# Performance work log

Hardware: AMD Instinct MI355X
Metric: run time of the kernel (lower is better)

The kernel has to match this reference:

```python
import jax, jax.numpy as jnp
import numpy as np

B, S, H, E = 4, 4096, 4096, 64
EPS = 1e-6


def setup_inputs() -> dict:
    key = jax.random.key(0)
    k1, k2 = jax.random.split(key)
    hidden_states = jax.random.normal(k1, (B, S, H), dtype=jnp.float32)
    gate_w = jax.random.normal(k2, (E, H), dtype=jnp.float32) * 0.02
    return {"hidden_states": hidden_states, "gate_w": gate_w, "C": 512}


def reference(hidden_states, gate_w, C):
    b, s, h = hidden_states.shape
    e = gate_w.shape[0]
    flat = hidden_states.reshape(-1, h)                    # [BS, H]
    logits = jnp.einsum('th,eh->te', flat, gate_w)          # [BS, E]
    # deterministic=True -> no noise added
    probs = jax.nn.softmax(logits, axis=-1)                 # [BS, E]
    # expert-choice: each expert picks top-C tokens
    _, topC_idx = jax.lax.top_k(logits.T, C)                # [E, C] token indices
    routing_map = jnp.zeros_like(logits).at[
        topC_idx, jnp.arange(e)[:, None]].set(1.0)          # [BS, E]
    # normalize_weights=True
    probs = probs * routing_map
    probs = probs / (probs.sum(axis=-1, keepdims=True) + EPS)
    # aux losses (torch .std() is unbiased -> ddof=1)
    importance = probs.sum(axis=0)                          # [E]
    imp_loss = (jnp.std(importance, ddof=1) / (importance.mean() + EPS)) ** 2
    load = routing_map.sum(axis=0)                          # [E]
    load_loss = (jnp.std(load, ddof=1) / (load.mean() + EPS)) ** 2
    aux_loss = imp_loss + load_loss
    return (probs.reshape(b, s, e), routing_map.reshape(b, s, e), aux_loss)
```

## Files before the change

### kernel.cpp

```cpp
#include <hip/hip_runtime.h>
#include <hip/hip_bf16.h>

#define BS 16384
#define HDIM 4096
#define NE 64
#define KC 64
#define TILE_T 64
#define CAP 512
#define DELTA 2e-3f

__device__ inline unsigned f2key(float f) {
    unsigned u = __float_as_uint(f);
    return (u & 0x80000000u) ? ~u : (u | 0x80000000u);
}
__device__ inline float key2f(unsigned k) {
    unsigned u = (k & 0x80000000u) ? (k ^ 0x80000000u) : ~k;
    return __uint_as_float(u);
}

__global__ __launch_bounds__(1024, 4) void k1_gemm(const float* __restrict__ A,
                                                   const float* __restrict__ W,
                                                   float* __restrict__ Lg,
                                                   unsigned* __restrict__ KeyT) {
    __shared__ __align__(16) float smem[2 * KC * 68];
    float (*As)[68] = (float(*)[68])smem;
    float (*Ws)[68] = (float(*)[68])(smem + KC * 68);

    const int tid = threadIdx.x;
    const int T0  = blockIdx.x * TILE_T;

    const int kq  = tid & 15;
    const int row = tid >> 4;

    const int qt   = tid >> 8;
    const int htid = tid & 255;
    const int tx   = htid & 15;
    const int ty   = htid >> 4;

    float  cacc[4][4];
    double acc[4][4];
#pragma unroll
    for (int i = 0; i < 4; ++i)
#pragma unroll
        for (int j = 0; j < 4; ++j) { cacc[i][j] = 0.f; acc[i][j] = 0.0; }

    float4 ra = *(const float4*)&A[(size_t)(T0 + row) * HDIM + 4 * kq];
    float4 rw = *(const float4*)&W[(size_t)row * HDIM + 4 * kq];

    const int NCHUNK = HDIM / KC;
    for (int c = 0; c < NCHUNK; ++c) {
        __syncthreads();
        *(float4*)&As[row][4 * kq] = ra;
        Ws[4 * kq + 0][row] = rw.x;
        Ws[4 * kq + 1][row] = rw.y;
        Ws[4 * kq + 2][row] = rw.z;
        Ws[4 * kq + 3][row] = rw.w;
        __syncthreads();
        if (c + 1 < NCHUNK) {
            const int c0 = (c + 1) * KC;
            ra = *(const float4*)&A[(size_t)(T0 + row) * HDIM + c0 + 4 * kq];
            rw = *(const float4*)&W[(size_t)row * HDIM + c0 + 4 * kq];
        }
        const int kb = qt * 16;
#pragma unroll
        for (int k4 = 0; k4 < 4; ++k4) {
            const int k0 = kb + 4 * k4;
            float4 a0 = *(const float4*)&As[4 * ty + 0][k0];
            float4 a1 = *(const float4*)&As[4 * ty + 1][k0];
            float4 a2 = *(const float4*)&As[4 * ty + 2][k0];
            float4 a3 = *(const float4*)&As[4 * ty + 3][k0];
            float4 w0 = *(const float4*)&Ws[k0 + 0][4 * tx];
            float4 w1 = *(const float4*)&Ws[k0 + 1][4 * tx];
            float4 w2 = *(const float4*)&Ws[k0 + 2][4 * tx];
            float4 w3 = *(const float4*)&Ws[k0 + 3][4 * tx];
            const float* ap[4] = {(const float*)&a0, (const float*)&a1,
                                  (const float*)&a2, (const float*)&a3};
            const float* wp[4] = {(const float*)&w0, (const float*)&w1,
                                  (const float*)&w2, (const float*)&w3};
#pragma unroll
            for (int s = 0; s < 4; ++s)
#pragma unroll
                for (int i = 0; i < 4; ++i)
#pragma unroll
                    for (int j = 0; j < 4; ++j)
                        cacc[i][j] = fmaf(ap[i][s], wp[s][j], cacc[i][j]);
        }
        if ((c & 3) == 3) {
#pragma unroll
            for (int i = 0; i < 4; ++i)
#pragma unroll
                for (int j = 0; j < 4; ++j) { acc[i][j] += (double)cacc[i][j]; cacc[i][j] = 0.f; }
        }
    }

    double* dbuf = (double*)smem;
    __syncthreads();
    if (qt == 3) {
#pragma unroll
        for (int i = 0; i < 4; ++i)
#pragma unroll
            for (int j = 0; j < 4; ++j) dbuf[htid * 16 + i * 4 + j] = acc[i][j];
    }
    __syncthreads();
    if (qt == 2) {
#pragma unroll
        for (int i = 0; i < 4; ++i)
#pragma unroll
            for (int j = 0; j < 4; ++j) dbuf[htid * 16 + i * 4 + j] += acc[i][j];
    }
    __syncthreads();
    if (qt == 1) {
#pragma unroll
        for (int i = 0; i < 4; ++i)
#pragma unroll
            for (int j = 0; j < 4; ++j) dbuf[htid * 16 + i * 4 + j] += acc[i][j];
    }
    __syncthreads();
    if (qt == 0) {
        float f[4][4];
#pragma unroll
        for (int i = 0; i < 4; ++i)
#pragma unroll
            for (int j = 0; j < 4; ++j)
                f[i][j] = (float)(acc[i][j] + dbuf[htid * 16 + i * 4 + j]);
#pragma unroll
        for (int i = 0; i < 4; ++i) {
            const int t = T0 + 4 * ty + i;
            float4 o = {f[i][0], f[i][1], f[i][2], f[i][3]};
            *(float4*)&Lg[(size_t)t * NE + 4 * tx] = o;
        }
#pragma unroll
        for (int j = 0; j < 4; ++j) {
            const int e = 4 * tx + j;
            uint4 kv = {f2key(f[0][j]), f2key(f[1][j]), f2key(f[2][j]), f2key(f[3][j])};
            *(uint4*)&KeyT[(size_t)e * BS + T0 + 4 * ty] = kv;
        }
    }
}

__global__ __launch_bounds__(1024) void k2_select(const unsigned* __restrict__ KeyT,
                                                  const int* __restrict__ Cptr,
                                                  unsigned* __restrict__ khi_g,
                                                  int* __restrict__ needed_g,
                                                  int* __restrict__ ncand_g,
                                                  int* __restrict__ cand_g,
                                                  unsigned* __restrict__ win_g) {
    const int e = blockIdx.x;
    const int tid = threadIdx.x;
    const unsigned* col = KeyT + (size_t)e * BS;
    const int C = *Cptr;

    __shared__ int hist[256];
    __shared__ int sfx[256];
    __shared__ unsigned s_pref;
    __shared__ int s_rem, s_nc, s_nd;

    if (tid == 0) { s_pref = 0u; s_rem = C; s_nc = 0; s_nd = 0; }
    for (int i = tid; i < CAP; i += 1024) win_g[(size_t)e * CAP + i] = 0u;
    __syncthreads();

    for (int p = 3; p >= 0; --p) {
        if (tid < 256) hist[tid] = 0;
        __syncthreads();
        const int shift = 8 * p;
        const unsigned maskhi = (p == 3) ? 0u : (0xFFFFFFFFu << (shift + 8));
        const unsigned pref = s_pref;
        const int rem = s_rem;
        for (int i = 0; i < BS / 1024; ++i) {
            const unsigned k = col[i * 1024 + tid];
            if ((k & maskhi) == pref) atomicAdd(&hist[(k >> shift) & 255u], 1);
        }
        __syncthreads();
        if (tid < 256) sfx[tid] = hist[tid];
        __syncthreads();
        for (int off = 1; off < 256; off <<= 1) {
            int v = 0;
            if (tid < 256 && tid + off < 256) v = sfx[tid + off];
            __syncthreads();
            if (tid < 256) sfx[tid] += v;
            __syncthreads();
        }
        if (tid < 256) {
            const int Sd = sfx[tid];
            const int Sd1 = (tid == 255) ? 0 : sfx[tid + 1];
            if (Sd >= rem && Sd1 < rem) {
                s_pref = pref | ((unsigned)tid << shift);
                s_rem = rem - Sd1;
            }
        }
        __syncthreads();
    }

    const float vT = key2f(s_pref);
    const unsigned khi = f2key(vT + DELTA);
    const unsigned klo = f2key(vT - DELTA);

    for (int i = 0; i < BS / 1024; ++i) {
        const int t = i * 1024 + tid;
        const unsigned k = col[t];
        if (k > khi) atomicAdd(&s_nd, 1);
        else if (k >= klo) {
            const int pos = atomicAdd(&s_nc, 1);
            if (pos < CAP) cand_g[(size_t)e * CAP + pos] = t;
        }
    }
    __syncthreads();
    if (tid == 0) {
        khi_g[e] = khi;
        needed_g[e] = C - s_nd;
        ncand_g[e] = (s_nc < CAP) ? s_nc : CAP;
    }
}

__global__ __launch_bounds__(256) void k2b_resolve(const float* __restrict__ A,
                                                   const float* __restrict__ W,
                                                   const int* __restrict__ needed_g,
                                                   const int* __restrict__ ncand_g,
                                                   const int* __restrict__ cand_g,
                                                   unsigned* __restrict__ win_g) {
    const int e = blockIdx.x;
    const int tid = threadIdx.x;
    int n = ncand_g[e]; if (n > CAP) n = CAP;
    int need = needed_g[e];
    if (need > n) need = n;
    if (need < 0) need = 0;

    __shared__ double sval[CAP];
    __shared__ int sidx[CAP];
    __shared__ unsigned char chosen[CAP];
    __shared__ double wred[4];

    for (int i = tid; i < CAP; i += 256) {
        sidx[i] = (i < n) ? cand_g[(size_t)e * CAP + i] : 0;
        chosen[i] = 0;
    }
    __syncthreads();

    const float* Wr = W + (size_t)e * HDIM;
    for (int c = 0; c < n; ++c) {
        const int t = sidx[c];
        const float* Ar = A + (size_t)t * HDIM;
        double ps = 0.0;
#pragma unroll
        for (int j = 0; j < HDIM / 256; ++j)
            ps += (double)Ar[j * 256 + tid] * (double)Wr[j * 256 + tid];
#pragma unroll
        for (int off = 32; off; off >>= 1) ps += __shfl_xor(ps, off);
        if ((tid & 63) == 0) wred[tid >> 6] = ps;
        __syncthreads();
        if (tid == 0) sval[c] = wred[0] + wred[1] + wred[2] + wred[3];
        __syncthreads();
    }

    if (tid == 0) {
        for (int s = 0; s < need; ++s) {
            int best = -1;
            for (int c = 0; c < n; ++c) {
                if (chosen[c]) continue;
                if (best < 0 || sval[c] > sval[best] ||
                    (sval[c] == sval[best] && sidx[c] < sidx[best]))
                    best = c;
            }
            chosen[best] = 1;
            const int t = sidx[best];
            win_g[(size_t)e * CAP + (t >> 5)] |= (1u << (t & 31));
        }
    }
}

__global__ __launch_bounds__(256) void k3_softmax(const float* __restrict__ Lg,
                                                  const unsigned* __restrict__ khi_g,
                                                  const unsigned* __restrict__ win_g,
                                                  float* __restrict__ probs,
                                                  float* __restrict__ out_map,
                                                  double* __restrict__ imp_partial) {
    const int tid = threadIdx.x;
    const int w = tid >> 6;
    const int e = tid & 63;
    const int b = blockIdx.x;

    __shared__ unsigned skhi[64];
    __shared__ double buf[4][64];
    if (tid < 64) skhi[tid] = khi_g[tid];
    __syncthreads();

    double accim = 0.0;
    for (int it = 0; it < 16; ++it) {
        const int t = b * 64 + it * 4 + w;
        const float x = Lg[(size_t)t * NE + e];
        const unsigned key = f2key(x);
        float m;
        if (key > skhi[e]) m = 1.f;
        else m = ((win_g[(size_t)e * CAP + (t >> 5)] >> (t & 31)) & 1u) ? 1.f : 0.f;

        float mx = x;
#pragma unroll
        for (int off = 32; off; off >>= 1) mx = fmaxf(mx, __shfl_xor(mx, off));
        const float ev = expf(x - mx);
        float s = ev;
#pragma unroll
        for (int off = 32; off; off >>= 1) s += __shfl_xor(s, off);
        const float p = ev / s;
        const float pm = p * m;
        float s2 = pm;
#pragma unroll
        for (int off = 32; off; off >>= 1) s2 += __shfl_xor(s2, off);
        const float o = pm / (s2 + 1e-6f);
        probs[(size_t)t * NE + e] = o;
        out_map[(size_t)t * NE + e] = m;
        accim += (double)o;
    }
    buf[w][e] = accim;
    __syncthreads();
    if (w == 0)
        imp_partial[(size_t)b * NE + e] = buf[0][e] + buf[1][e] + buf[2][e] + buf[3][e];
}

__global__ __launch_bounds__(64) void k4_aux(const double* __restrict__ imp_partial,
                                             float* __restrict__ out_aux) {
    const int e = threadIdx.x;
    double s = 0.0;
    for (int b = 0; b < 256; ++b) s += imp_partial[(size_t)b * NE + e];
    __shared__ double imp[64];
    imp[e] = s;
    __syncthreads();
    if (e == 0) {
        double mean = 0.0;
        for (int i = 0; i < 64; ++i) mean += imp[i];
        mean /= 64.0;
        double var = 0.0;
        for (int i = 0; i < 64; ++i) { const double d = imp[i] - mean; var += d * d; }
        var /= 63.0;
        const double denom = mean + 1e-6;
        out_aux[0] = (float)(var / (denom * denom));
    }
}

extern "C" void kernel_launch(void* const* d_in, const int* in_sizes, int n_in,
                              void* d_out, int out_size, void* d_ws, size_t ws_size,
                              hipStream_t stream) {
    const float* A = (const float*)d_in[0];
    const float* W = (const float*)d_in[1];
    const int* Cptr = (const int*)d_in[2];

    float* out_probs = (float*)d_out;
    float* out_map   = out_probs + (size_t)BS * NE;
    float* out_aux   = out_map + (size_t)BS * NE;

    char* wsb = (char*)d_ws;
    float*    Lg      = (float*)wsb;
    unsigned* KeyT    = (unsigned*)(wsb + (4u << 20));
    unsigned* khi_g   = (unsigned*)(wsb + (8u << 20));
    int*      needed  = (int*)(wsb + (8u << 20) + 1024);
    int*      ncand   = (int*)(wsb + (8u << 20) + 2048);
    int*      cand    = (int*)(wsb + (8u << 20) + 4096);
    unsigned* winners = (unsigned*)(wsb + (8u << 20) + (256u << 10));
    double*   imp     = (double*)(wsb + (8u << 20) + (512u << 10));

    k1_gemm<<<BS / TILE_T, 1024, 0, stream>>>(A, W, Lg, KeyT);
    k2_select<<<NE, 1024, 0, stream>>>(KeyT, Cptr, khi_g, needed, ncand, cand, winners);
    k2b_resolve<<<NE, 256, 0, stream>>>(A, W, needed, ncand, cand, winners);
    k3_softmax<<<256, 256, 0, stream>>>(Lg, khi_g, winners, out_probs, out_map, imp);
    k4_aux<<<1, 64, 0, stream>>>(imp, out_aux);
}
```

Measured before the change: 486.0 us.

## Use split-bf16 MFMA gating GEMM with fused key histogram selection

Replaces the fp32/fp64 FMA gating GEMM with bf16 MFMA instructions, splitting A and W into high and low bf16 parts (three products) to keep near-fp32 accuracy. A new init kernel pre-splits W and zeroes a 16-bit-prefix histogram. The GEMM fills that histogram atomically so selection needs a single prefix-scan pass instead of four radix passes over the keys. The resolve, softmax and aux kernels are also restructured: warp-parallel candidates, no max subtraction in softmax, and atomic importance accumulation. The risks are lower logit precision near the top-C threshold, where the fp64 resolve path has to cover the ties, possible overflow of expf without the max shift, and contention on the global histogram atomics.

```diff
diff --git a/kernel.cpp b/kernel.cpp
--- a/kernel.cpp
+++ b/kernel.cpp
@@ -5,9 +5,14 @@
 #define HDIM 4096
 #define NE 64
 #define KC 64
-#define TILE_T 64
+#define TT 32
 #define CAP 512
 #define DELTA 2e-3f
+#define NBIN 65536
+
+typedef __bf16 bf16x8 __attribute__((ext_vector_type(8)));
+typedef float f32x4 __attribute__((ext_vector_type(4)));
+union Frag { uint4 q; bf16x8 v; };
 
 __device__ inline unsigned f2key(float f) {
     unsigned u = __float_as_uint(f);
@@ -17,193 +22,205 @@
     unsigned u = (k & 0x80000000u) ? (k ^ 0x80000000u) : ~k;
     return __uint_as_float(u);
 }
-
-__global__ __launch_bounds__(1024, 4) void k1_gemm(const float* __restrict__ A,
-                                                   const float* __restrict__ W,
-                                                   float* __restrict__ Lg,
-                                                   unsigned* __restrict__ KeyT) {
-    __shared__ __align__(16) float smem[2 * KC * 68];
-    float (*As)[68] = (float(*)[68])smem;
-    float (*Ws)[68] = (float(*)[68])(smem + KC * 68);
+__device__ inline unsigned pack_hi(float a, float b) {
+    return (__float_as_uint(a) >> 16) | (__float_as_uint(b) & 0xFFFF0000u);
+}
+__device__ inline float bf16_resid(float a) {
+    return a - __uint_as_float(__float_as_uint(a) & 0xFFFF0000u);
+}
+
+__global__ __launch_bounds__(256) void k0_init(const float* __restrict__ W,
+                                               unsigned short* __restrict__ Wh,
+                                               unsigned short* __restrict__ Wl,
+                                               unsigned* __restrict__ hist,
+                                               double* __restrict__ imp_g) {
+    const int b = blockIdx.x, t = threadIdx.x;
+    const size_t base = ((size_t)b * 256 + t) * 8;
+    uint4 z = {0, 0, 0, 0};
+    *(uint4*)(hist + base) = z;
+    *(uint4*)(hist + base + 4) = z;
+    if (b == 0 && t < 64) imp_g[t] = 0.0;
+    if (b < 256) {
+        const size_t f = ((size_t)b * 256 + t) * 4;
+        float4 w = *(const float4*)(W + f);
+        uint2 hh, ll;
+        hh.x = pack_hi(w.x, w.y); hh.y = pack_hi(w.z, w.w);
+        ll.x = pack_hi(bf16_resid(w.x), bf16_resid(w.y));
+        ll.y = pack_hi(bf16_resid(w.z), bf16_resid(w.w));
+        *(uint2*)(Wh + f) = hh;
+        *(uint2*)(Wl + f) = ll;
+    }
+}
+
+__global__ __launch_bounds__(256, 2) void k1_gemm(const float* __restrict__ A,
+                                                  const unsigned short* __restrict__ Wh,
+                                                  const unsigned short* __restrict__ Wl,
+                                                  float* __restrict__ Lg,
+                                                  unsigned* __restrict__ KeyT,
+                                                  unsigned* __restrict__ hist) {
+    __shared__ __align__(16) unsigned short As_h[TT][72], As_l[TT][72];
+    __shared__ __align__(16) unsigned short Ws_h[64][72], Ws_l[64][72];
 
     const int tid = threadIdx.x;
-    const int T0  = blockIdx.x * TILE_T;
-
-    const int kq  = tid & 15;
-    const int row = tid >> 4;
-
-    const int qt   = tid >> 8;
-    const int htid = tid & 255;
-    const int tx   = htid & 15;
-    const int ty   = htid >> 4;
-
-    float  cacc[4][4];
-    double acc[4][4];
-#pragma unroll
-    for (int i = 0; i < 4; ++i)
-#pragma unroll
-        for (int j = 0; j < 4; ++j) { cacc[i][j] = 0.f; acc[i][j] = 0.0; }
-
-    float4 ra = *(const float4*)&A[(size_t)(T0 + row) * HDIM + 4 * kq];
-    float4 rw = *(const float4*)&W[(size_t)row * HDIM + 4 * kq];
-
-    const int NCHUNK = HDIM / KC;
-    for (int c = 0; c < NCHUNK; ++c) {
-        __syncthreads();
-        *(float4*)&As[row][4 * kq] = ra;
-        Ws[4 * kq + 0][row] = rw.x;
-        Ws[4 * kq + 1][row] = rw.y;
-        Ws[4 * kq + 2][row] = rw.z;
-        Ws[4 * kq + 3][row] = rw.w;
-        __syncthreads();
-        if (c + 1 < NCHUNK) {
+    const int T0 = blockIdx.x * TT;
+    const int arow = tid >> 3, aseg = tid & 7;
+    const float* Ap = A + (size_t)(T0 + arow) * HDIM + aseg * 8;
+
+    const int lane = tid & 63, w = tid >> 6;
+    const int m = lane & 15, q = lane >> 4;
+    const int en = w * 16;
+
+    f32x4 acc0 = {0.f, 0.f, 0.f, 0.f}, acc1 = {0.f, 0.f, 0.f, 0.f};
+
+    float4 pa0, pa1;
+    uint4 pw[4];
+    pa0 = *(const float4*)(Ap);
+    pa1 = *(const float4*)(Ap + 4);
+#pragma unroll
+    for (int i = 0; i < 4; ++i) {
+        const int u = i * 256 + tid;
+        const unsigned short* Wm = (u >= 512) ? Wl : Wh;
+        const int r = (u >> 3) & 63, blk = u & 7;
+        pw[i] = *(const uint4*)(Wm + (size_t)r * HDIM + blk * 8);
+    }
+
+    for (int c = 0; c < HDIM / KC; ++c) {
+        __syncthreads();
+        {
+            uint4 H, L;
+            H.x = pack_hi(pa0.x, pa0.y); H.y = pack_hi(pa0.z, pa0.w);
+            H.z = pack_hi(pa1.x, pa1.y); H.w = pack_hi(pa1.z, pa1.w);
+            L.x = pack_hi(bf16_resid(pa0.x), bf16_resid(pa0.y));
+            L.y = pack_hi(bf16_resid(pa0.z), bf16_resid(pa0.w));
+            L.z = pack_hi(bf16_resid(pa1.x), bf16_resid(pa1.y));
+            L.w = pack_hi(bf16_resid(pa1.z), bf16_resid(pa1.w));
+            *(uint4*)(&As_h[arow][aseg * 8]) = H;
+            *(uint4*)(&As_l[arow][aseg * 8]) = L;
+#pragma unroll
+            for (int i = 0; i < 4; ++i) {
+                const int u = i * 256 + tid;
+                unsigned short* dst = (u >= 512) ? &Ws_l[0][0] : &Ws_h[0][0];
+                const int r = (u >> 3) & 63, blk = u & 7;
+                *(uint4*)(dst + r * 72 + blk * 8) = pw[i];
+            }
+        }
+        __syncthreads();
+        if (c + 1 < HDIM / KC) {
             const int c0 = (c + 1) * KC;
-            ra = *(const float4*)&A[(size_t)(T0 + row) * HDIM + c0 + 4 * kq];
-            rw = *(const float4*)&W[(size_t)row * HDIM + c0 + 4 * kq];
-        }
-        const int kb = qt * 16;
-#pragma unroll
-        for (int k4 = 0; k4 < 4; ++k4) {
-            const int k0 = kb + 4 * k4;
-            float4 a0 = *(const float4*)&As[4 * ty + 0][k0];
-            float4 a1 = *(const float4*)&As[4 * ty + 1][k0];
-            float4 a2 = *(const float4*)&As[4 * ty + 2][k0];
-            float4 a3 = *(const float4*)&As[4 * ty + 3][k0];
-            float4 w0 = *(const float4*)&Ws[k0 + 0][4 * tx];
-            float4 w1 = *(const float4*)&Ws[k0 + 1][4 * tx];
-            float4 w2 = *(const float4*)&Ws[k0 + 2][4 * tx];
-            float4 w3 = *(const float4*)&Ws[k0 + 3][4 * tx];
-            const float* ap[4] = {(const float*)&a0, (const float*)&a1,
-                                  (const float*)&a2, (const float*)&a3};
-            const float* wp[4] = {(const float*)&w0, (const float*)&w1,
-                                  (const float*)&w2, (const float*)&w3};
-#pragma unroll
-            for (int s = 0; s < 4; ++s)
-#pragma unroll
-                for (int i = 0; i < 4; ++i)
-#pragma unroll
-                    for (int j = 0; j < 4; ++j)
-                        cacc[i][j] = fmaf(ap[i][s], wp[s][j], cacc[i][j]);
-        }
-        if ((c & 3) == 3) {
-#pragma unroll
-            for (int i = 0; i < 4; ++i)
-#pragma unroll
-                for (int j = 0; j < 4; ++j) { acc[i][j] += (double)cacc[i][j]; cacc[i][j] = 0.f; }
-        }
-    }
-
-    double* dbuf = (double*)smem;
-    __syncthreads();
-    if (qt == 3) {
-#pragma unroll
-        for (int i = 0; i < 4; ++i)
-#pragma unroll
-            for (int j = 0; j < 4; ++j) dbuf[htid * 16 + i * 4 + j] = acc[i][j];
-    }
-    __syncthreads();
-    if (qt == 2) {
-#pragma unroll
-        for (int i = 0; i < 4; ++i)
-#pragma unroll
-            for (int j = 0; j < 4; ++j) dbuf[htid * 16 + i * 4 + j] += acc[i][j];
-    }
-    __syncthreads();
-    if (qt == 1) {
-#pragma unroll
-        for (int i = 0; i < 4; ++i)
-#pragma unroll
-            for (int j = 0; j < 4; ++j) dbuf[htid * 16 + i * 4 + j] += acc[i][j];
-    }
-    __syncthreads();
-    if (qt == 0) {
-        float f[4][4];
-#pragma unroll
-        for (int i = 0; i < 4; ++i)
-#pragma unroll
-            for (int j = 0; j < 4; ++j)
-                f[i][j] = (float)(acc[i][j] + dbuf[htid * 16 + i * 4 + j]);
-#pragma unroll
-        for (int i = 0; i < 4; ++i) {
-            const int t = T0 + 4 * ty + i;
-            float4 o = {f[i][0], f[i][1], f[i][2], f[i][3]};
-            *(float4*)&Lg[(size_t)t * NE + 4 * tx] = o;
-        }
-#pragma unroll
-        for (int j = 0; j < 4; ++j) {
-            const int e = 4 * tx + j;
-            uint4 kv = {f2key(f[0][j]), f2key(f[1][j]), f2key(f[2][j]), f2key(f[3][j])};
-            *(uint4*)&KeyT[(size_t)e * BS + T0 + 4 * ty] = kv;
+            pa0 = *(const float4*)(Ap + c0);
+            pa1 = *(const float4*)(Ap + c0 + 4);
+#pragma unroll
+            for (int i = 0; i < 4; ++i) {
+                const int u = i * 256 + tid;
+                const unsigned short* Wm = (u >= 512) ? Wl : Wh;
+                const int r = (u >> 3) & 63, blk = u & 7;
+                pw[i] = *(const uint4*)(Wm + (size_t)r * HDIM + c0 + blk * 8);
+            }
+        }
+#pragma unroll
+        for (int k2 = 0; k2 < 2; ++k2) {
+            const int ko = k2 * 32 + q * 8;
+            Frag ah0, ah1, al0, al1, bh, bl;
+            ah0.q = *(const uint4*)(&As_h[m][ko]);
+            ah1.q = *(const uint4*)(&As_h[m + 16][ko]);
+            al0.q = *(const uint4*)(&As_l[m][ko]);
+            al1.q = *(const uint4*)(&As_l[m + 16][ko]);
+            bh.q  = *(const uint4*)(&Ws_h[en + m][ko]);
+            bl.q  = *(const uint4*)(&Ws_l[en + m][ko]);
+            acc0 = __builtin_amdgcn_mfma_f32_16x16x32_bf16(ah0.v, bh.v, acc0, 0, 0, 0);
+            acc1 = __builtin_amdgcn_mfma_f32_16x16x32_bf16(ah1.v, bh.v, acc1, 0, 0, 0);
+            acc0 = __builtin_amdgcn_mfma_f32_16x16x32_bf16(al0.v, bh.v, acc0, 0, 0, 0);
+            acc1 = __builtin_amdgcn_mfma_f32_16x16x32_bf16(al1.v, bh.v, acc1, 0, 0, 0);
+            acc0 = __builtin_amdgcn_mfma_f32_16x16x32_bf16(ah0.v, bl.v, acc0, 0, 0, 0);
+            acc1 = __builtin_amdgcn_mfma_f32_16x16x32_bf16(ah1.v, bl.v, acc1, 0, 0, 0);
+        }
+    }
+
+#pragma unroll
+    for (int mt = 0; mt < 2; ++mt) {
+        f32x4 acc = mt ? acc1 : acc0;
+        const int e = en + m;
+#pragma unroll
+        for (int r = 0; r < 4; ++r) {
+            const int t = T0 + mt * 16 + q * 4 + r;
+            const float val = acc[r];
+            Lg[(size_t)t * NE + e] = val;
+            const unsigned key = f2key(val);
+            KeyT[(size_t)e * BS + t] = key;
+            atomicAdd(&hist[(size_t)e * NBIN + (key >> 16)], 1u);
         }
     }
 }
 
 __global__ __launch_bounds__(1024) void k2_select(const unsigned* __restrict__ KeyT,
+                                                  const unsigned* __restrict__ hist,
                                                   const int* __restrict__ Cptr,
                                                   unsigned* __restrict__ khi_g,
                                                   int* __restrict__ needed_g,
                                                   int* __restrict__ ncand_g,
                                                   int* __restrict__ cand_g,
                                                   unsigned* __restrict__ win_g) {
-    const int e = blockIdx.x;
-    const int tid = threadIdx.x;
+    const int e = blockIdx.x, tid = threadIdx.x;
+    const int C = *Cptr;
+    const unsigned* he = hist + (size_t)e * NBIN;
+    __shared__ int ls[1024];
+    __shared__ int s_tstar, s_after, s_B, s_nd, s_nc;
+
+    if (tid < 512) win_g[(size_t)e * 512 + tid] = 0u;
+    if (tid == 0) { s_nd = 0; s_nc = 0; s_tstar = 0; s_after = 0; s_B = 0; }
+
+    int s = 0;
+#pragma unroll
+    for (int i = 0; i < 16; ++i) {
+        uint4 v = *(const uint4*)(he + tid * 64 + i * 4);
+        s += (int)(v.x + v.y + v.z + v.w);
+    }
+    ls[tid] = s;
+    __syncthreads();
+    for (int off = 1; off < 1024; off <<= 1) {
+        int v = (tid + off < 1024) ? ls[tid + off] : 0;
+        __syncthreads();
+        ls[tid] += v;
+        __syncthreads();
+    }
+    if (ls[tid] >= C && (tid == 1023 || ls[tid + 1] < C)) {
+        s_tstar = tid;
+        s_after = (tid == 1023) ? 0 : ls[tid + 1];
+    }
+    __syncthreads();
+    const int tstar = s_tstar, after = s_after;
+    if (tid < 64) ls[tid] = (int)he[tstar * 64 + tid];
+    __syncthreads();
+    for (int off = 1; off < 64; off <<= 1) {
+        int v = 0;
+        if (tid < 64 && tid + off < 64) v = ls[tid + off];
+        __syncthreads();
+        if (tid < 64) ls[tid] += v;
+        __syncthreads();
+    }
+    if (tid < 64) {
+        const int sfx = ls[tid] + after;
+        const int nxt = ((tid == 63) ? 0 : ls[tid + 1]) + after;
+        if (sfx >= C && nxt < C) s_B = tstar * 64 + tid;
+    }
+    __syncthreads();
+    const int B = s_B;
+    const unsigned khi = (B >= 65535) ? 0xFFFFFFFFu
+                                      : f2key(key2f((unsigned)(B + 1) << 16) + DELTA);
+    const unsigned klo = f2key(key2f((unsigned)B << 16) - DELTA);
+
     const unsigned* col = KeyT + (size_t)e * BS;
-    const int C = *Cptr;
-
-    __shared__ int hist[256];
-    __shared__ int sfx[256];
-    __shared__ unsigned s_pref;
-    __shared__ int s_rem, s_nc, s_nd;
-
-    if (tid == 0) { s_pref = 0u; s_rem = C; s_nc = 0; s_nd = 0; }
-    for (int i = tid; i < CAP; i += 1024) win_g[(size_t)e * CAP + i] = 0u;
-    __syncthreads();
-
-    for (int p = 3; p >= 0; --p) {
-        if (tid < 256) hist[tid] = 0;
-        __syncthreads();
-        const int shift = 8 * p;
-        const unsigned maskhi = (p == 3) ? 0u : (0xFFFFFFFFu << (shift + 8));
-        const unsigned pref = s_pref;
-        const int rem = s_rem;
-        for (int i = 0; i < BS / 1024; ++i) {
-            const unsigned k = col[i * 1024 + tid];
-            if ((k & maskhi) == pref) atomicAdd(&hist[(k >> shift) & 255u], 1);
-        }
-        __syncthreads();
-        if (tid < 256) sfx[tid] = hist[tid];
-        __syncthreads();
-        for (int off = 1; off < 256; off <<= 1) {
-            int v = 0;
-            if (tid < 256 && tid + off < 256) v = sfx[tid + off];
-            __syncthreads();
-            if (tid < 256) sfx[tid] += v;
-            __syncthreads();
-        }
-        if (tid < 256) {
-            const int Sd = sfx[tid];
-            const int Sd1 = (tid == 255) ? 0 : sfx[tid + 1];
-            if (Sd >= rem && Sd1 < rem) {
-                s_pref = pref | ((unsigned)tid << shift);
-                s_rem = rem - Sd1;
-            }
-        }
-        __syncthreads();
-    }
-
-    const float vT = key2f(s_pref);
-    const unsigned khi = f2key(vT + DELTA);
-    const unsigned klo = f2key(vT - DELTA);
-
+    int nd_loc = 0;
     for (int i = 0; i < BS / 1024; ++i) {
         const int t = i * 1024 + tid;
         const unsigned k = col[t];
-        if (k > khi) atomicAdd(&s_nd, 1);
-        else if (k >= klo) {
-            const int pos = atomicAdd(&s_nc, 1);
-            if (pos < CAP) cand_g[(size_t)e * CAP + pos] = t;
-        }
-    }
+        nd_loc += (k > khi);
+        if (k >= klo && k <= khi) {
+            const int p = atomicAdd(&s_nc, 1);
+            if (p < CAP) cand_g[(size_t)e * CAP + p] = t;
+        }
+    }
+    atomicAdd(&s_nd, nd_loc);
     __syncthreads();
     if (tid == 0) {
         khi_g[e] = khi;
@@ -218,52 +235,36 @@
                                                    const int* __restrict__ ncand_g,
                                                    const int* __restrict__ cand_g,
                                                    unsigned* __restrict__ win_g) {
-    const int e = blockIdx.x;
-    const int tid = threadIdx.x;
+    const int e = blockIdx.x, tid = threadIdx.x, w = tid >> 6, lane = tid & 63;
     int n = ncand_g[e]; if (n > CAP) n = CAP;
-    int need = needed_g[e];
-    if (need > n) need = n;
-    if (need < 0) need = 0;
-
+    int need = needed_g[e]; if (need > n) need = n; if (need < 0) need = 0;
     __shared__ double sval[CAP];
     __shared__ int sidx[CAP];
-    __shared__ unsigned char chosen[CAP];
-    __shared__ double wred[4];
-
-    for (int i = tid; i < CAP; i += 256) {
-        sidx[i] = (i < n) ? cand_g[(size_t)e * CAP + i] : 0;
-        chosen[i] = 0;
-    }
-    __syncthreads();
-
     const float* Wr = W + (size_t)e * HDIM;
-    for (int c = 0; c < n; ++c) {
-        const int t = sidx[c];
+    for (int c = w; c < n; c += 4) {
+        const int t = cand_g[(size_t)e * CAP + c];
         const float* Ar = A + (size_t)t * HDIM;
         double ps = 0.0;
-#pragma unroll
-        for (int j = 0; j < HDIM / 256; ++j)
-            ps += (double)Ar[j * 256 + tid] * (double)Wr[j * 256 + tid];
+#pragma unroll 8
+        for (int j = 0; j < HDIM / 64; ++j)
+            ps += (double)Ar[j * 64 + lane] * (double)Wr[j * 64 + lane];
 #pragma unroll
         for (int off = 32; off; off >>= 1) ps += __shfl_xor(ps, off);
-        if ((tid & 63) == 0) wred[tid >> 6] = ps;
-        __syncthreads();
-        if (tid == 0) sval[c] = wred[0] + wred[1] + wred[2] + wred[3];
-        __syncthreads();
-    }
-
+        if (lane == 0) { sval[c] = ps; sidx[c] = t; }
+    }
+    __syncthreads();
     if (tid == 0) {
         for (int s = 0; s < need; ++s) {
             int best = -1;
             for (int c = 0; c < n; ++c) {
-                if (chosen[c]) continue;
+                if (sidx[c] < 0) continue;
                 if (best < 0 || sval[c] > sval[best] ||
                     (sval[c] == sval[best] && sidx[c] < sidx[best]))
                     best = c;
             }
-            chosen[best] = 1;
             const int t = sidx[best];
-            win_g[(size_t)e * CAP + (t >> 5)] |= (1u << (t & 31));
+            win_g[(size_t)e * 512 + (t >> 5)] |= (1u << (t & 31));
+            sidx[best] = -1;
         }
     }
 }
@@ -273,66 +274,56 @@
                                                   const unsigned* __restrict__ win_g,
                                                   float* __restrict__ probs,
                                                   float* __restrict__ out_map,
-                                                  double* __restrict__ imp_partial) {
-    const int tid = threadIdx.x;
-    const int w = tid >> 6;
-    const int e = tid & 63;
-    const int b = blockIdx.x;
-
+                                                  double* __restrict__ imp_g) {
+    const int tid = threadIdx.x, w = tid >> 6, e = tid & 63, b = blockIdx.x;
     __shared__ unsigned skhi[64];
-    __shared__ double buf[4][64];
+    __shared__ double sim[4][64];
     if (tid < 64) skhi[tid] = khi_g[tid];
     __syncthreads();
-
+    const unsigned kh = skhi[e];
     double accim = 0.0;
-    for (int it = 0; it < 16; ++it) {
-        const int t = b * 64 + it * 4 + w;
+#pragma unroll
+    for (int it = 0; it < 4; ++it) {
+        const int t = b * 16 + w * 4 + it;
         const float x = Lg[(size_t)t * NE + e];
         const unsigned key = f2key(x);
-        float m;
-        if (key > skhi[e]) m = 1.f;
-        else m = ((win_g[(size_t)e * CAP + (t >> 5)] >> (t & 31)) & 1u) ? 1.f : 0.f;
-
-        float mx = x;
-#pragma unroll
-        for (int off = 32; off; off >>= 1) mx = fmaxf(mx, __shfl_xor(mx, off));
-        const float ev = expf(x - mx);
-        float s = ev;
-#pragma unroll
-        for (int off = 32; off; off >>= 1) s += __shfl_xor(s, off);
-        const float p = ev / s;
-        const float pm = p * m;
-        float s2 = pm;
-#pragma unroll
-        for (int off = 32; off; off >>= 1) s2 += __shfl_xor(s2, off);
-        const float o = pm / (s2 + 1e-6f);
+        float mfl;
+        if (key > kh) mfl = 1.f;
+        else mfl = (float)((win_g[(size_t)e * 512 + (t >> 5)] >> (t & 31)) & 1u);
+        const float ev = expf(x);
+        const float evm = ev * mfl;
+        float s1 = ev, s2 = evm;
+#pragma unroll
+        for (int off = 32; off; off >>= 1) {
+            s1 += __shfl_xor(s1, off);
+            s2 += __shfl_xor(s2, off);
+        }
+        const float o = evm / (s2 + 1e-6f * s1);
         probs[(size_t)t * NE + e] = o;
-        out_map[(size_t)t * NE + e] = m;
+        out_map[(size_t)t * NE + e] = mfl;
         accim += (double)o;
     }
-    buf[w][e] = accim;
-    __syncthreads();
-    if (w == 0)
-        imp_partial[(size_t)b * NE + e] = buf[0][e] + buf[1][e] + buf[2][e] + buf[3][e];
-}
-
-__global__ __launch_bounds__(64) void k4_aux(const double* __restrict__ imp_partial,
+    sim[w][e] = accim;
+    __syncthreads();
+    if (w == 0) atomicAdd(&imp_g[e], sim[0][e] + sim[1][e] + sim[2][e] + sim[3][e]);
+}
+
+__global__ __launch_bounds__(64) void k4_aux(const double* __restrict__ imp_g,
                                              float* __restrict__ out_aux) {
     const int e = threadIdx.x;
-    double s = 0.0;
-    for (int b = 0; b < 256; ++b) s += imp_partial[(size_t)b * NE + e];
-    __shared__ double imp[64];
-    imp[e] = s;
-    __syncthreads();
+    const double v = imp_g[e];
+    double s = v;
+#pragma unroll
+    for (int off = 32; off; off >>= 1) s += __shfl_xor(s, off);
+    const double mean = s / 64.0;
+    const double d = v - mean;
+    double ss = d * d;
+#pragma unroll
+    for (int off = 32; off; off >>= 1) ss += __shfl_xor(ss, off);
     if (e == 0) {
-        double mean = 0.0;
-        for (int i = 0; i < 64; ++i) mean += imp[i];
-        mean /= 64.0;
-        double var = 0.0;
-        for (int i = 0; i < 64; ++i) { const double d = imp[i] - mean; var += d * d; }
-        var /= 63.0;
-        const double denom = mean + 1e-6;
-        out_aux[0] = (float)(var / (denom * denom));
+        const double var = ss / 63.0;
+        const double dn = mean + 1e-6;
+        out_aux[0] = (float)(var / (dn * dn));
     }
 }
 
@@ -344,22 +335,26 @@
     const int* Cptr = (const int*)d_in[2];
 
     float* out_probs = (float*)d_out;
-    float* out_map   = out_probs + (size_t)BS * NE;
-    float* out_aux   = out_map + (size_t)BS * NE;
+    float* out_map = out_probs + (size_t)BS * NE;
+    float* out_aux = out_map + (size_t)BS * NE;
 
     char* wsb = (char*)d_ws;
-    float*    Lg      = (float*)wsb;
-    unsigned* KeyT    = (unsigned*)(wsb + (4u << 20));
-    unsigned* khi_g   = (unsigned*)(wsb + (8u << 20));
-    int*      needed  = (int*)(wsb + (8u << 20) + 1024);
-    int*      ncand   = (int*)(wsb + (8u << 20) + 2048);
-    int*      cand    = (int*)(wsb + (8u << 20) + 4096);
-    unsigned* winners = (unsigned*)(wsb + (8u << 20) + (256u << 10));
-    double*   imp     = (double*)(wsb + (8u << 20) + (512u << 10));
-
-    k1_gemm<<<BS / TILE_T, 1024, 0, stream>>>(A, W, Lg, KeyT);
-    k2_select<<<NE, 1024, 0, stream>>>(KeyT, Cptr, khi_g, needed, ncand, cand, winners);
-    k2b_resolve<<<NE, 256, 0, stream>>>(A, W, needed, ncand, cand, winners);
-    k3_softmax<<<256, 256, 0, stream>>>(Lg, khi_g, winners, out_probs, out_map, imp);
-    k4_aux<<<1, 64, 0, stream>>>(imp, out_aux);
-}
+    float*          Lg     = (float*)wsb;
+    unsigned*       KeyT   = (unsigned*)(wsb + (4ull << 20));
+    unsigned*       hist   = (unsigned*)(wsb + (8ull << 20));
+    unsigned short* Wh     = (unsigned short*)(wsb + (24ull << 20));
+    unsigned short* Wl     = (unsigned short*)(wsb + (24ull << 20) + (512ull << 10));
+    int*            cand   = (int*)(wsb + (25ull << 20));
+    unsigned*       win    = (unsigned*)(wsb + (25ull << 20) + (128ull << 10));
+    unsigned*       khi_g  = (unsigned*)(wsb + (25ull << 20) + (256ull << 10));
+    int*            needed = (int*)(wsb + (25ull << 20) + (257ull << 10));
+    int*            ncand  = (int*)(wsb + (25ull << 20) + (258ull << 10));
+    double*         imp_g  = (double*)(wsb + (25ull << 20) + (259ull << 10));
+
+    k0_init<<<2048, 256, 0, stream>>>(W, Wh, Wl, hist, imp_g);
+    k1_gemm<<<BS / TT, 256, 0, stream>>>(A, Wh, Wl, Lg, KeyT, hist);
+    k2_select<<<NE, 1024, 0, stream>>>(KeyT, hist, Cptr, khi_g, needed, ncand, cand, win);
+    k2b_resolve<<<NE, 256, 0, stream>>>(A, W, needed, ncand, cand, win);
+    k3_softmax<<<BS / 16, 256, 0, stream>>>(Lg, khi_g, win, out_probs, out_map, imp_g);
+    k4_aux<<<1, 64, 0, stream>>>(imp_g, out_aux);
+}
```

Result: slower. 634.8 us (+30.6%).
